# Optimization experiments

Measured on AMD Instinct MI355X. Metric: run time of the kernel, lower is better.

Reference implementation:

```python
import jax, jax.numpy as jnp
import numpy as np

B, T, C = 64, 2048, 32
OUT_T = 2048

def setup_inputs() -> dict:
    key = jax.random.key(0)
    k1, k2 = jax.random.split(key)
    X = jax.random.normal(k1, (B, T, C), dtype=jnp.float32)
    # small init so deformations are modest displacements, like a trained locnet
    W_loc = jax.random.normal(k2, (T * C, OUT_T), dtype=jnp.float32) * 1e-3
    b_loc = jnp.zeros((OUT_T,), dtype=jnp.float32)
    return {"X": X, "W_loc": W_loc, "b_loc": b_loc}

def reference(X, W_loc, b_loc):
    b, t, c = X.shape
    out_t = W_loc.shape[1]
    # localization net: flatten + dense -> per-output-point displacement (B, OUT_T)
    deformation = X.reshape(b, t * c) @ W_loc + b_loc
    # sampling grid: linspace(0, T-1, OUT_T), shared across batch, shifted by deformation
    grid = jnp.linspace(0.0, jnp.float32(t - 1), out_t)  # (OUT_T,)
    x = grid[None, :] + deformation                       # (B, OUT_T) float sample coords
    # linear interpolation with clamped integer neighbors
    x0 = jnp.floor(x).astype(jnp.int32)
    x1 = x0 + 1
    x0c = jnp.clip(x0, 0, t - 1)
    x1c = jnp.clip(x1, 0, t - 1)
    batch_idx = jnp.arange(b)[:, None]                    # (B, 1)
    v0 = X[batch_idx, x0c]                                # (B, OUT_T, C) gather along T
    v1 = X[batch_idx, x1c]                                # (B, OUT_T, C)
    # weights use the CLIPPED coords cast back to float (faithful to original)
    w0 = (x1c.astype(x.dtype) - x)[..., None]             # (B, OUT_T, 1)
    w1 = (x - x0c.astype(x.dtype))[..., None]
    return w0 * v0 + w1 * v1                              # (B, OUT_T, C)
```

## Files before the change

kernel.cpp:

```cpp
#include <hip/hip_runtime.h>
#include <hip/hip_bf16.h>
#include <stdint.h>

constexpr int BATCH = 64;
constexpr int T     = 2048;
constexpr int CCH   = 32;
constexpr int OUT_T = 2048;
constexpr int K     = T * CCH;
constexpr int N     = OUT_T;

constexpr int TN     = 64;
constexpr int NBN    = N / TN;
constexpr int KSPLIT = 64;
constexpr int CK     = K / KSPLIT;
constexpr int BK     = 32;
constexpr int NS     = CK / BK;
constexpr int NWG    = NBN * KSPLIT;

typedef __attribute__((ext_vector_type(8))) short short8;
typedef __attribute__((ext_vector_type(4))) float f32x4;

__device__ __forceinline__ void split2t(float a, float b, unsigned& hpk, unsigned& lpk) {
  unsigned ua = __float_as_uint(a), ub = __float_as_uint(b);
  hpk = (ua >> 16) | (ub & 0xFFFF0000u);
  float la = a - __uint_as_float(ua & 0xFFFF0000u);
  float lb = b - __uint_as_float(ub & 0xFFFF0000u);
  __hip_bfloat162 l2 = __float22bfloat162_rn(make_float2(la, lb));
  __builtin_memcpy(&lpk, &l2, 4);
}

__global__ __launch_bounds__(256) void xsplit_kernel(
    const float* __restrict__ X, ushort* __restrict__ Xhi, ushort* __restrict__ Xlo) {
  const int i = blockIdx.x * 256 + threadIdx.x;
  const float4 v = ((const float4*)X)[i];
  unsigned h01, l01, h23, l23;
  split2t(v.x, v.y, h01, l01);
  split2t(v.z, v.w, h23, l23);
  uint2 hv; hv.x = h01; hv.y = h23;
  uint2 lv; lv.x = l01; lv.y = l23;
  ((uint2*)Xhi)[i] = hv;
  ((uint2*)Xlo)[i] = lv;
}

__global__ __launch_bounds__(256) void gemm_flat_kernel(
    const ushort* __restrict__ Xhi,
    const ushort* __restrict__ Xlo,
    const float*  __restrict__ W,
    float* __restrict__ def) {
  const int bid = blockIdx.x;
  const int lb  = (bid & 7) * (NWG / 8) + (bid >> 3);
  const int bn  = lb & (NBN - 1);
  const int bk  = lb >> 5;

  const int tid  = threadIdx.x;
  const int lane = tid & 63;
  const int wave = tid >> 6;
  const int r = lane & 15;
  const int g = lane >> 4;

  const int kbase = bk * CK;
  const int ncol  = bn * TN + wave * 16 + r;

  const float* wbase = W + (size_t)(kbase + 8 * g) * N + ncol;

  f32x4 acc[4] = {};
  float b0[8], b1[8], b2[8], b3[8];
  short8 a0h[4], a0l[4], a1h[4], a1l[4];

  auto issueB = [&](int t, float (&bb)[8]) {
    const float* p = wbase + (size_t)t * (BK * N);
#pragma unroll
    for (int j = 0; j < 8; ++j) bb[j] = p[(size_t)j * N];
  };

  auto issueA = [&](int t, short8 (&ah)[4], short8 (&al)[4]) {
    const unsigned off = (unsigned)(((size_t)r * K + kbase + t * BK + 8 * g) * 2);
#pragma unroll
    for (int mf = 0; mf < 4; ++mf) {
      ah[mf] = *(const short8*)((const char*)Xhi + off + (size_t)mf * (16 * K * 2));
      al[mf] = *(const short8*)((const char*)Xlo + off + (size_t)mf * (16 * K * 2));
    }
  };

  auto domfma = [&](float (&bb)[8], short8 (&ah)[4], short8 (&al)[4]) {
    union { short8 s; unsigned u[4]; } bh, bl;
#pragma unroll
    for (int p2 = 0; p2 < 4; ++p2)
      split2t(bb[2 * p2], bb[2 * p2 + 1], bh.u[p2], bl.u[p2]);
#pragma unroll
    for (int mf = 0; mf < 4; ++mf) {
      acc[mf] = __builtin_amdgcn_mfma_f32_16x16x32_bf16(ah[mf], bh.s, acc[mf], 0, 0, 0);
      acc[mf] = __builtin_amdgcn_mfma_f32_16x16x32_bf16(ah[mf], bl.s, acc[mf], 0, 0, 0);
      acc[mf] = __builtin_amdgcn_mfma_f32_16x16x32_bf16(al[mf], bh.s, acc[mf], 0, 0, 0);
    }
  };

  issueB(0, b0); issueB(1, b1); issueB(2, b2); issueB(3, b3);
  issueA(0, a0h, a0l); issueA(1, a1h, a1l);

  for (int t = 0; t < NS - 4; t += 4) {
    domfma(b0, a0h, a0l); issueB(t + 4, b0); issueA(t + 2, a0h, a0l);
    domfma(b1, a1h, a1l); issueB(t + 5, b1); issueA(t + 3, a1h, a1l);
    domfma(b2, a0h, a0l); issueB(t + 6, b2); issueA(t + 4, a0h, a0l);
    domfma(b3, a1h, a1l); issueB(t + 7, b3); issueA(t + 5, a1h, a1l);
  }
  domfma(b0, a0h, a0l); issueA(30, a0h, a0l);
  domfma(b1, a1h, a1l); issueA(31, a1h, a1l);
  domfma(b2, a0h, a0l);
  domfma(b3, a1h, a1l);

#pragma unroll
  for (int mf = 0; mf < 4; ++mf) {
    const int mbase = mf * 16 + g * 4;
#pragma unroll
    for (int q = 0; q < 4; ++q) {
      atomicAdd(&def[(size_t)(mbase + q) * N + ncol], acc[mf][q]);
    }
  }
}

__global__ __launch_bounds__(256) void resample_kernel(
    const float* __restrict__ X,
    const float* __restrict__ def,
    const float* __restrict__ b_loc,
    float* __restrict__ out) {
  const int tid = blockIdx.x * 256 + threadIdx.x;
  const int c4 = tid & 7;
  const int o  = (tid >> 3) & (OUT_T - 1);
  const int b  = tid >> 14;

  const float x = (float)o + def[b * OUT_T + o] + b_loc[o];
  const float xf = floorf(x);
  const int x0 = (int)xf;
  const int x1 = x0 + 1;
  const int x0c = min(max(x0, 0), T - 1);
  const int x1c = min(max(x1, 0), T - 1);
  const float w0 = (float)x1c - x;
  const float w1 = x - (float)x0c;

  const float4 v0 = *(const float4*)&X[((size_t)b * T + x0c) * CCH + c4 * 4];
  const float4 v1 = *(const float4*)&X[((size_t)b * T + x1c) * CCH + c4 * 4];
  float4 res;
  res.x = w0 * v0.x + w1 * v1.x;
  res.y = w0 * v0.y + w1 * v1.y;
  res.z = w0 * v0.z + w1 * v1.z;
  res.w = w0 * v0.w + w1 * v1.w;
  *(float4*)&out[((size_t)b * OUT_T + o) * CCH + c4 * 4] = res;
}

extern "C" void kernel_launch(void* const* d_in, const int* in_sizes, int n_in,
                              void* d_out, int out_size, void* d_ws, size_t ws_size,
                              hipStream_t stream) {
  const float* X     = (const float*)d_in[0];
  const float* W     = (const float*)d_in[1];
  const float* b_loc = (const float*)d_in[2];
  float* out = (float*)d_out;

  float*  def = (float*)d_ws;
  ushort* Xhi = (ushort*)((char*)d_ws + (1u << 20));
  ushort* Xlo = (ushort*)((char*)d_ws + (1u << 20) + (size_t)BATCH * K * 2);

  hipMemsetAsync(def, 0, (size_t)BATCH * N * sizeof(float), stream);

  xsplit_kernel<<<(BATCH * K / 4) / 256, 256, 0, stream>>>(X, Xhi, Xlo);

  gemm_flat_kernel<<<NWG, 256, 0, stream>>>(Xhi, Xlo, W, def);

  resample_kernel<<<(BATCH * OUT_T * 8) / 256, 256, 0, stream>>>(X, def, b_loc, out);
}
```

Before: 883.1 us.

## Stage split W tiles in LDS and split M across waves

The GEMM kernel now loads each W element once per workgroup, splits it into bf16 hi/lo in registers, and stores the pieces to double-buffered shared memory. Each wave takes a 16-row M slice and reads all four N fragments from LDS. Previously every wave loaded all of A and split its own W columns. This removes redundant W splitting and A loads across waves, at the cost of LDS traffic and a __syncthreads per k-step.

```diff
diff --git a/kernel.cpp b/kernel.cpp
--- a/kernel.cpp
+++ b/kernel.cpp
@@ -42,7 +42,7 @@
   ((uint2*)Xlo)[i] = lv;
 }
 
-__global__ __launch_bounds__(256) void gemm_flat_kernel(
+__global__ __launch_bounds__(256) void gemm_kernel(
     const ushort* __restrict__ Xhi,
     const ushort* __restrict__ Xlo,
     const float*  __restrict__ W,
@@ -58,63 +58,96 @@
   const int r = lane & 15;
   const int g = lane >> 4;
 
+  __shared__ ushort Bhi[2][64][40];
+  __shared__ ushort Blo[2][64][40];
+
+  f32x4 acc[4] = {};
   const int kbase = bk * CK;
-  const int ncol  = bn * TN + wave * 16 + r;
-
-  const float* wbase = W + (size_t)(kbase + 8 * g) * N + ncol;
-
-  f32x4 acc[4] = {};
-  float b0[8], b1[8], b2[8], b3[8];
-  short8 a0h[4], a0l[4], a1h[4], a1l[4];
-
-  auto issueB = [&](int t, float (&bb)[8]) {
-    const float* p = wbase + (size_t)t * (BK * N);
-#pragma unroll
-    for (int j = 0; j < 8; ++j) bb[j] = p[(size_t)j * N];
-  };
-
-  auto issueA = [&](int t, short8 (&ah)[4], short8 (&al)[4]) {
-    const unsigned off = (unsigned)(((size_t)r * K + kbase + t * BK + 8 * g) * 2);
-#pragma unroll
-    for (int mf = 0; mf < 4; ++mf) {
-      ah[mf] = *(const short8*)((const char*)Xhi + off + (size_t)mf * (16 * K * 2));
-      al[mf] = *(const short8*)((const char*)Xlo + off + (size_t)mf * (16 * K * 2));
+
+  const char* aBaseH = (const char*)Xhi + ((size_t)(wave * 16 + r) * K + kbase + 8 * g) * 2;
+  const char* aBaseL = (const char*)Xlo + ((size_t)(wave * 16 + r) * K + kbase + 8 * g) * 2;
+
+  const int nW  = tid & 63;
+  const int kq0 = tid >> 6;
+  const float* wBase = W + (size_t)(kbase + kq0 * 4) * N + bn * TN + nW;
+
+  float  w0[8], w1[8], w2[8];
+  short8 a0h, a0l, a1h, a1l, a2h, a2l;
+
+  auto issueW = [&](int t, float (&s)[8]) {
+    const float* p = wBase + (size_t)t * BK * N;
+#pragma unroll
+    for (int j = 0; j < 4; ++j) {
+      s[j]     = p[(size_t)j * N];
+      s[4 + j] = p[(size_t)(16 + j) * N];
     }
   };
 
-  auto domfma = [&](float (&bb)[8], short8 (&ah)[4], short8 (&al)[4]) {
-    union { short8 s; unsigned u[4]; } bh, bl;
-#pragma unroll
-    for (int p2 = 0; p2 < 4; ++p2)
-      split2t(bb[2 * p2], bb[2 * p2 + 1], bh.u[p2], bl.u[p2]);
-#pragma unroll
-    for (int mf = 0; mf < 4; ++mf) {
-      acc[mf] = __builtin_amdgcn_mfma_f32_16x16x32_bf16(ah[mf], bh.s, acc[mf], 0, 0, 0);
-      acc[mf] = __builtin_amdgcn_mfma_f32_16x16x32_bf16(ah[mf], bl.s, acc[mf], 0, 0, 0);
-      acc[mf] = __builtin_amdgcn_mfma_f32_16x16x32_bf16(al[mf], bh.s, acc[mf], 0, 0, 0);
+  auto issueA = [&](int t, short8& ah, short8& al) {
+    ah = *(const short8*)(aBaseH + (size_t)t * BK * 2);
+    al = *(const short8*)(aBaseL + (size_t)t * BK * 2);
+  };
+
+  auto stageB = [&](int buf, float (&s)[8]) {
+    unsigned h01, l01, h23, l23;
+    split2t(s[0], s[1], h01, l01);
+    split2t(s[2], s[3], h23, l23);
+    uint2 hv; hv.x = h01; hv.y = h23;
+    uint2 lv; lv.x = l01; lv.y = l23;
+    *(uint2*)&Bhi[buf][nW][kq0 * 4] = hv;
+    *(uint2*)&Blo[buf][nW][kq0 * 4] = lv;
+    split2t(s[4], s[5], h01, l01);
+    split2t(s[6], s[7], h23, l23);
+    uint2 hv2; hv2.x = h01; hv2.y = h23;
+    uint2 lv2; lv2.x = l01; lv2.y = l23;
+    *(uint2*)&Bhi[buf][nW][(kq0 + 4) * 4] = hv2;
+    *(uint2*)&Blo[buf][nW][(kq0 + 4) * 4] = lv2;
+  };
+
+  auto mfma_step = [&](int buf, short8& ah, short8& al) {
+#pragma unroll
+    for (int f = 0; f < 4; ++f) {
+      short8 bh = *(const short8*)&Bhi[buf][f * 16 + r][g * 8];
+      short8 bl = *(const short8*)&Blo[buf][f * 16 + r][g * 8];
+      acc[f] = __builtin_amdgcn_mfma_f32_16x16x32_bf16(ah, bh, acc[f], 0, 0, 0);
+      acc[f] = __builtin_amdgcn_mfma_f32_16x16x32_bf16(ah, bl, acc[f], 0, 0, 0);
+      acc[f] = __builtin_amdgcn_mfma_f32_16x16x32_bf16(al, bh, acc[f], 0, 0, 0);
     }
   };
 
-  issueB(0, b0); issueB(1, b1); issueB(2, b2); issueB(3, b3);
+  auto dostep = [&](int t, float (&wsNext)[8], float (&wsStage)[8],
+                    short8& ahC, short8& alC, short8& ahN, short8& alN, int buf) {
+    if (t + 3 < NS) issueW(t + 3, wsNext);
+    if (t + 2 < NS) issueA(t + 2, ahN, alN);
+    mfma_step(buf, ahC, alC);
+    if (t + 1 < NS) stageB(buf ^ 1, wsStage);
+    __syncthreads();
+  };
+
+  issueW(0, w0); issueW(1, w1); issueW(2, w2);
   issueA(0, a0h, a0l); issueA(1, a1h, a1l);
-
-  for (int t = 0; t < NS - 4; t += 4) {
-    domfma(b0, a0h, a0l); issueB(t + 4, b0); issueA(t + 2, a0h, a0l);
-    domfma(b1, a1h, a1l); issueB(t + 5, b1); issueA(t + 3, a1h, a1l);
-    domfma(b2, a0h, a0l); issueB(t + 6, b2); issueA(t + 4, a0h, a0l);
-    domfma(b3, a1h, a1l); issueB(t + 7, b3); issueA(t + 5, a1h, a1l);
+  stageB(0, w0);
+  __syncthreads();
+
+#pragma unroll
+  for (int tb = 0; tb < 30; tb += 6) {
+    dostep(tb + 0, w0, w1, a0h, a0l, a2h, a2l, 0);
+    dostep(tb + 1, w1, w2, a1h, a1l, a0h, a0l, 1);
+    dostep(tb + 2, w2, w0, a2h, a2l, a1h, a1l, 0);
+    dostep(tb + 3, w0, w1, a0h, a0l, a2h, a2l, 1);
+    dostep(tb + 4, w1, w2, a1h, a1l, a0h, a0l, 0);
+    dostep(tb + 5, w2, w0, a2h, a2l, a1h, a1l, 1);
   }
-  domfma(b0, a0h, a0l); issueA(30, a0h, a0l);
-  domfma(b1, a1h, a1l); issueA(31, a1h, a1l);
-  domfma(b2, a0h, a0l);
-  domfma(b3, a1h, a1l);
-
-#pragma unroll
-  for (int mf = 0; mf < 4; ++mf) {
-    const int mbase = mf * 16 + g * 4;
+  dostep(30, w0, w1, a0h, a0l, a2h, a2l, 0);
+  dostep(31, w1, w2, a1h, a1l, a0h, a0l, 1);
+
+  const int mrow = wave * 16 + g * 4;
+#pragma unroll
+  for (int f = 0; f < 4; ++f) {
+    const int ncol = bn * TN + f * 16 + r;
 #pragma unroll
     for (int q = 0; q < 4; ++q) {
-      atomicAdd(&def[(size_t)(mbase + q) * N + ncol], acc[mf][q]);
+      atomicAdd(&def[(size_t)(mrow + q) * N + ncol], acc[f][q]);
     }
   }
 }
@@ -164,7 +197,7 @@
 
   xsplit_kernel<<<(BATCH * K / 4) / 256, 256, 0, stream>>>(X, Xhi, Xlo);
 
-  gemm_flat_kernel<<<NWG, 256, 0, stream>>>(Xhi, Xlo, W, def);
+  gemm_kernel<<<NWG, 256, 0, stream>>>(Xhi, Xlo, W, def);
 
   resample_kernel<<<(BATCH * OUT_T * 8) / 256, 256, 0, stream>>>(X, def, b_loc, out);
 }
```

Result: faster. 734.2 us (-16.9%).
